# Performance work log

Measured on AMD Instinct MI355X. Metric: run time of the kernel, lower is better.

Reference implementation:

```python
import jax, jax.numpy as jnp
import numpy as np

MAXLEN = 256          # max per-graph segment length (static for jit)
SOFT_LABEL_NUM = 4    # hardcoded in the original module
B = 512               # num_graphs


def setup_inputs() -> dict:
    key = jax.random.key(0)
    k1, k2, k3 = jax.random.split(key, 3)
    # ragged per-graph lengths in [2, MAXLEN]; >=2 so the original's
    # length-1 skip path (and its cursor bug) never triggers
    s_num = jax.random.randint(k1, (B,), 2, MAXLEN + 1, dtype=jnp.int32)
    T = int(jnp.sum(s_num))
    logits = jax.random.normal(k2, (T,), dtype=jnp.float32)
    labels = jax.random.randint(k3, (T,), 0, SOFT_LABEL_NUM, dtype=jnp.int32)
    return {"logits": logits, "labels": labels, "s_num": s_num}


def reference(logits, labels, s_num):
    T = logits.shape[0]
    ends = jnp.cumsum(s_num)
    offsets = ends - s_num                                   # segment starts
    pos_in_seg = jnp.arange(MAXLEN)
    idx = jnp.clip(offsets[:, None] + pos_in_seg[None, :], 0, T - 1)  # [B, L]
    tok_mask = pos_in_seg[None, :] < s_num[:, None]                    # [B, L]

    lg = logits[idx]                                   # [B, L] padded logits
    lb = labels[idx]                                   # [B, L] padded labels

    # pairwise logsigmoid(pos - neg), computed once for all soft labels
    ls = jax.nn.log_sigmoid(lg[:, :, None] - lg[:, None, :])  # [B, L, L]

    means, valids = [], []
    for s in range(1, SOFT_LABEL_NUM):
        pos = (tok_mask & (lb == s)).astype(lg.dtype)  # [B, L]
        neg = (tok_mask & (lb < s)).astype(lg.dtype)   # [B, L]
        npos = pos.sum(-1)                             # [B]
        nneg = neg.sum(-1)                             # [B]
        pair_sum = jnp.einsum('bp,bpn,bn->b', pos, ls, neg)
        valid = (npos > 0) & (nneg > 0)
        mean_s = jnp.where(valid, pair_sum / jnp.maximum(npos * nneg, 1.0), 0.0)
        means.append(mean_s)
        valids.append(valid)

    means = jnp.stack(means)                 # [3, B]
    valids = jnp.stack(valids)               # [3, B]
    cnt = valids.astype(lg.dtype).sum(0)     # valid soft-label count per graph
    graph_valid = (s_num > 1) & (cnt > 0)
    graph_lp = jnp.where(graph_valid, means.sum(0) / jnp.maximum(cnt, 1.0), 0.0)
    n_valid = jnp.maximum(graph_valid.astype(lg.dtype).sum(), 1.0)
    loss = -(graph_lp.sum() / n_valid)
    return loss
```

## Files before the change

### kernel.cpp

```cpp
#include <hip/hip_runtime.h>
#include <hip/hip_bf16.h>


__global__ __launch_bounds__(256) void bpr_main(const float* __restrict__ logits,
                                                const int* __restrict__ labels,
                                                const int* __restrict__ s_num,
                                                int B,
                                                float* __restrict__ glp,
                                                float* __restrict__ flg) {
    const int b = blockIdx.x;
    const int t = threadIdx.x;

    __shared__ __align__(16) float se[256];
    __shared__ float sx[256];
    __shared__ float psum[4];
    __shared__ int   cnt[4];
    __shared__ int   cur[4];
    __shared__ int   wsum[4];

    if (t < 4) { psum[t] = 0.0f; cnt[t] = 0; cur[t] = 0; }
    se[t] = 0.0f;
    sx[t] = 0.0f;

    int partial = 0;
    for (int i = t; i < b; i += 256) partial += s_num[i];
    #pragma unroll
    for (int off = 32; off > 0; off >>= 1)
        partial += __shfl_down(partial, off, 64);
    if ((t & 63) == 0) wsum[t >> 6] = partial;
    __syncthreads();
    const int offset = wsum[0] + wsum[1] + wsum[2] + wsum[3];
    const int L = s_num[b];

    float x = 0.0f;
    int   l = 0;
    if (t < L) {
        x = logits[offset + t];
        l = labels[offset + t];
        atomicAdd(&cnt[l], 1);
    }
    __syncthreads();

    const int c0 = cnt[0], c1 = cnt[1], c2 = cnt[2];
    const int P1 = c0, P2 = c0 + c1, P3 = c0 + c1 + c2;

    if (t < L) {
        const int base = (l == 1) ? P1 : (l == 2) ? P2 : (l == 3) ? P3 : 0;
        const int pos  = base + atomicAdd(&cur[l], 1);
        se[pos] = __expf(x);
        sx[pos] = x;
    }
    __syncthreads();

    int si = 0;
    if (t < L) si = (t >= P1) + (t >= P2) + (t >= P3);
    const int C = (si == 1) ? P1 : (si == 2) ? P2 : (si == 3) ? P3 : 0;

    const float xi = sx[t];
    const float Ei = se[t];
    float acc2 = 0.0f;
    for (int j = 0; j < C; j += 8) {
        const float4 e0 = *reinterpret_cast<const float4*>(&se[j]);
        const float4 e1 = *reinterpret_cast<const float4*>(&se[j + 4]);
        acc2 += (j + 0 < C) ? __log2f(Ei + e0.x) : 0.0f;
        acc2 += (j + 1 < C) ? __log2f(Ei + e0.y) : 0.0f;
        acc2 += (j + 2 < C) ? __log2f(Ei + e0.z) : 0.0f;
        acc2 += (j + 3 < C) ? __log2f(Ei + e0.w) : 0.0f;
        acc2 += (j + 4 < C) ? __log2f(Ei + e1.x) : 0.0f;
        acc2 += (j + 5 < C) ? __log2f(Ei + e1.y) : 0.0f;
        acc2 += (j + 6 < C) ? __log2f(Ei + e1.z) : 0.0f;
        acc2 += (j + 7 < C) ? __log2f(Ei + e1.w) : 0.0f;
    }

    if (si > 0) {
        const float a = (float)C * xi - 0.69314718055994531f * acc2;
        atomicAdd(&psum[si], a);
    }
    __syncthreads();

    if (t == 0) {
        const int P[4] = {0, P1, P2, P3};
        float lp = 0.0f;
        int   c  = 0;
        #pragma unroll
        for (int s = 1; s < 4; ++s) {
            const int npos = cnt[s];
            const int nneg = P[s];
            if (npos > 0 && nneg > 0) {
                lp += psum[s] / ((float)npos * (float)nneg);
                ++c;
            }
        }
        const bool gv = (c > 0);
        glp[b] = gv ? lp / (float)c : 0.0f;
        flg[b] = gv ? 1.0f : 0.0f;
    }
}

__global__ __launch_bounds__(256) void bpr_reduce(const float* __restrict__ glp,
                                                  const float* __restrict__ flg,
                                                  int B, float* __restrict__ out) {
    const int t = threadIdx.x;
    float s = 0.0f, n = 0.0f;
    for (int i = t; i < B; i += 256) { s += glp[i]; n += flg[i]; }
    #pragma unroll
    for (int off = 32; off > 0; off >>= 1) {
        s += __shfl_down(s, off, 64);
        n += __shfl_down(n, off, 64);
    }
    __shared__ float ws[4], wn[4];
    if ((t & 63) == 0) { ws[t >> 6] = s; wn[t >> 6] = n; }
    __syncthreads();
    if (t == 0) {
        const float S = ws[0] + ws[1] + ws[2] + ws[3];
        const float N = wn[0] + wn[1] + wn[2] + wn[3];
        out[0] = -(S / fmaxf(N, 1.0f));
    }
}

extern "C" void kernel_launch(void* const* d_in, const int* in_sizes, int n_in,
                              void* d_out, int out_size, void* d_ws, size_t ws_size,
                              hipStream_t stream) {
    const float* logits = (const float*)d_in[0];
    const int*   labels = (const int*)d_in[1];
    const int*   s_num  = (const int*)d_in[2];
    const int B = in_sizes[2];

    float* glp = (float*)d_ws;
    float* flg = glp + B;

    bpr_main<<<B, 256, 0, stream>>>(logits, labels, s_num, B, glp, flg);
    bpr_reduce<<<1, 256, 0, stream>>>(glp, flg, B, (float*)d_out);
}
```

Measured before the change: 14.28 us.

## Split pairwise loop across four thread slices and use ballot-based label bucketing

Launches each graph block with 1024 threads so four 256-thread slices share the inner negative loop in a strided way, cutting per-thread serial log2 work. Shared-memory atomics for label counts and slot assignment are replaced by wave ballots and popcounts, and per-label partial sums are reduced with wave shuffles before one atomic per wave. The final reduce kernel reads with float4 loads. The larger blocks add barrier cost and reduce how many blocks fit per CU. Correctness depends on the rank-based slot order, and the stale shared entries past L are no longer zeroed.

```diff
diff --git a/kernel.cpp b/kernel.cpp
--- a/kernel.cpp
+++ b/kernel.cpp
@@ -2,97 +2,115 @@
 #include <hip/hip_bf16.h>
 
 
-__global__ __launch_bounds__(256) void bpr_main(const float* __restrict__ logits,
-                                                const int* __restrict__ labels,
-                                                const int* __restrict__ s_num,
-                                                int B,
-                                                float* __restrict__ glp,
-                                                float* __restrict__ flg) {
-    const int b = blockIdx.x;
-    const int t = threadIdx.x;
+__global__ __launch_bounds__(1024) void bpr_main(const float* __restrict__ logits,
+                                                 const int* __restrict__ labels,
+                                                 const int* __restrict__ s_num,
+                                                 int B,
+                                                 float* __restrict__ glp,
+                                                 float* __restrict__ flg) {
+    const int b  = blockIdx.x;
+    const int t  = threadIdx.x;
+    const int r  = t & 255;
+    const int sl = t >> 8;
+    const int w  = t >> 6;
+    const int lane = t & 63;
 
     __shared__ __align__(16) float se[256];
     __shared__ float sx[256];
     __shared__ float psum[4];
-    __shared__ int   cnt[4];
-    __shared__ int   cur[4];
+    __shared__ int   wcnt[4][4];
     __shared__ int   wsum[4];
 
-    if (t < 4) { psum[t] = 0.0f; cnt[t] = 0; cur[t] = 0; }
-    se[t] = 0.0f;
-    sx[t] = 0.0f;
+    if (t < 4) psum[t] = 0.0f;
 
-    int partial = 0;
-    for (int i = t; i < b; i += 256) partial += s_num[i];
-    #pragma unroll
-    for (int off = 32; off > 0; off >>= 1)
-        partial += __shfl_down(partial, off, 64);
-    if ((t & 63) == 0) wsum[t >> 6] = partial;
+    if (t < 256) {
+        int partial = 0;
+        for (int i = t; i < b; i += 256) partial += s_num[i];
+        #pragma unroll
+        for (int off = 32; off > 0; off >>= 1)
+            partial += __shfl_down(partial, off, 64);
+        if (lane == 0) wsum[w] = partial;
+    }
     __syncthreads();
     const int offset = wsum[0] + wsum[1] + wsum[2] + wsum[3];
     const int L = s_num[b];
 
     float x = 0.0f;
-    int   l = 0;
-    if (t < L) {
+    int   l = -1;
+    if (t < 256 && t < L) {
         x = logits[offset + t];
         l = labels[offset + t];
-        atomicAdd(&cnt[l], 1);
     }
+    const unsigned long long m0 = __ballot(l == 0);
+    const unsigned long long m1 = __ballot(l == 1);
+    const unsigned long long m2 = __ballot(l == 2);
+    const unsigned long long m3 = __ballot(l == 3);
+    if (w < 4 && lane == 0) {
+        wcnt[w][0] = __popcll(m0);
+        wcnt[w][1] = __popcll(m1);
+        wcnt[w][2] = __popcll(m2);
+        wcnt[w][3] = __popcll(m3);
+    }
+    const unsigned long long below = lane ? (~0ull >> (64 - lane)) : 0ull;
+    const unsigned long long mymask = (l == 0) ? m0 : (l == 1) ? m1 : (l == 2) ? m2 : m3;
+    const int rank = __popcll(mymask & below);
     __syncthreads();
 
-    const int c0 = cnt[0], c1 = cnt[1], c2 = cnt[2];
+    int c0 = wcnt[0][0] + wcnt[1][0] + wcnt[2][0] + wcnt[3][0];
+    int c1 = wcnt[0][1] + wcnt[1][1] + wcnt[2][1] + wcnt[3][1];
+    int c2 = wcnt[0][2] + wcnt[1][2] + wcnt[2][2] + wcnt[3][2];
+    int c3 = wcnt[0][3] + wcnt[1][3] + wcnt[2][3] + wcnt[3][3];
     const int P1 = c0, P2 = c0 + c1, P3 = c0 + c1 + c2;
 
-    if (t < L) {
-        const int base = (l == 1) ? P1 : (l == 2) ? P2 : (l == 3) ? P3 : 0;
-        const int pos  = base + atomicAdd(&cur[l], 1);
+    if (t < 256 && t < L) {
+        int base = (l == 0) ? 0 : (l == 1) ? P1 : (l == 2) ? P2 : P3;
+        for (int w2 = 0; w2 < w; ++w2) base += wcnt[w2][l];
+        const int pos = base + rank;
         se[pos] = __expf(x);
         sx[pos] = x;
     }
     __syncthreads();
 
     int si = 0;
-    if (t < L) si = (t >= P1) + (t >= P2) + (t >= P3);
+    if (r < L) si = (r >= P1) + (r >= P2) + (r >= P3);
     const int C = (si == 1) ? P1 : (si == 2) ? P2 : (si == 3) ? P3 : 0;
+    const float xi = sx[r];
+    const float Ei = se[r];
 
-    const float xi = sx[t];
-    const float Ei = se[t];
     float acc2 = 0.0f;
-    for (int j = 0; j < C; j += 8) {
+    for (int j = 8 * sl; j + 8 <= C; j += 32) {
         const float4 e0 = *reinterpret_cast<const float4*>(&se[j]);
         const float4 e1 = *reinterpret_cast<const float4*>(&se[j + 4]);
-        acc2 += (j + 0 < C) ? __log2f(Ei + e0.x) : 0.0f;
-        acc2 += (j + 1 < C) ? __log2f(Ei + e0.y) : 0.0f;
-        acc2 += (j + 2 < C) ? __log2f(Ei + e0.z) : 0.0f;
-        acc2 += (j + 3 < C) ? __log2f(Ei + e0.w) : 0.0f;
-        acc2 += (j + 4 < C) ? __log2f(Ei + e1.x) : 0.0f;
-        acc2 += (j + 5 < C) ? __log2f(Ei + e1.y) : 0.0f;
-        acc2 += (j + 6 < C) ? __log2f(Ei + e1.z) : 0.0f;
-        acc2 += (j + 7 < C) ? __log2f(Ei + e1.w) : 0.0f;
+        acc2 += __log2f(Ei + e0.x) + __log2f(Ei + e0.y)
+              + __log2f(Ei + e0.z) + __log2f(Ei + e0.w)
+              + __log2f(Ei + e1.x) + __log2f(Ei + e1.y)
+              + __log2f(Ei + e1.z) + __log2f(Ei + e1.w);
     }
+    const int jb = C & ~7;
+    if (si > 0 && sl == ((C >> 3) & 3)) {
+        for (int j = jb; j < C; ++j) acc2 += __log2f(Ei + se[j]);
+    }
+    float v = -0.69314718055994531f * acc2;
+    if (sl == 0 && si > 0) v += (float)C * xi;
 
-    if (si > 0) {
-        const float a = (float)C * xi - 0.69314718055994531f * acc2;
-        atomicAdd(&psum[si], a);
+    #pragma unroll
+    for (int s2 = 1; s2 < 4; ++s2) {
+        float val = (si == s2) ? v : 0.0f;
+        #pragma unroll
+        for (int off = 32; off > 0; off >>= 1)
+            val += __shfl_down(val, off, 64);
+        if (lane == 0 && val != 0.0f) atomicAdd(&psum[s2], val);
     }
     __syncthreads();
 
     if (t == 0) {
-        const int P[4] = {0, P1, P2, P3};
         float lp = 0.0f;
-        int   c  = 0;
-        #pragma unroll
-        for (int s = 1; s < 4; ++s) {
-            const int npos = cnt[s];
-            const int nneg = P[s];
-            if (npos > 0 && nneg > 0) {
-                lp += psum[s] / ((float)npos * (float)nneg);
-                ++c;
-            }
-        }
-        const bool gv = (c > 0);
-        glp[b] = gv ? lp / (float)c : 0.0f;
+        int   cc = 0;
+        if (c1 > 0 && P1 > 0) { lp += psum[1] / ((float)c1 * (float)P1); ++cc; }
+        if (c2 > 0 && P2 > 0) { lp += psum[2] / ((float)c2 * (float)P2); ++cc; }
+        if (c3 > 0 && P3 > 0) { lp += psum[3] / ((float)c3 * (float)P3); ++cc; }
+        const bool gv = (cc > 0);
+        glp[b] = gv ? lp / (float)cc : 0.0f;
         flg[b] = gv ? 1.0f : 0.0f;
     }
 }
@@ -101,19 +119,29 @@
                                                   const float* __restrict__ flg,
                                                   int B, float* __restrict__ out) {
     const int t = threadIdx.x;
+    const int lane = t & 63;
+    const int w = t >> 6;
+    const int n4 = B >> 2;
     float s = 0.0f, n = 0.0f;
-    for (int i = t; i < B; i += 256) { s += glp[i]; n += flg[i]; }
+    if (t < 128) {
+        const float4* g4 = (const float4*)glp;
+        for (int i = t; i < n4; i += 128) { float4 v = g4[i]; s += v.x + v.y + v.z + v.w; }
+        if (t == 0)   for (int i = n4 << 2; i < B; ++i) s += glp[i];
+    } else {
+        const float4* f4 = (const float4*)flg;
+        for (int i = t - 128; i < n4; i += 128) { float4 v = f4[i]; n += v.x + v.y + v.z + v.w; }
+        if (t == 128) for (int i = n4 << 2; i < B; ++i) n += flg[i];
+    }
+    float val = s + n;
     #pragma unroll
-    for (int off = 32; off > 0; off >>= 1) {
-        s += __shfl_down(s, off, 64);
-        n += __shfl_down(n, off, 64);
-    }
-    __shared__ float ws[4], wn[4];
-    if ((t & 63) == 0) { ws[t >> 6] = s; wn[t >> 6] = n; }
+    for (int off = 32; off > 0; off >>= 1)
+        val += __shfl_down(val, off, 64);
+    __shared__ float wred[4];
+    if (lane == 0) wred[w] = val;
     __syncthreads();
     if (t == 0) {
-        const float S = ws[0] + ws[1] + ws[2] + ws[3];
-        const float N = wn[0] + wn[1] + wn[2] + wn[3];
+        const float S = wred[0] + wred[1];
+        const float N = wred[2] + wred[3];
         out[0] = -(S / fmaxf(N, 1.0f));
     }
 }
@@ -129,6 +157,6 @@
     float* glp = (float*)d_ws;
     float* flg = glp + B;
 
-    bpr_main<<<B, 256, 0, stream>>>(logits, labels, s_num, B, glp, flg);
+    bpr_main<<<B, 1024, 0, stream>>>(logits, labels, s_num, B, glp, flg);
     bpr_reduce<<<1, 256, 0, stream>>>(glp, flg, B, (float*)d_out);
 }
```

Measured after the change: 13.81 us. 3.3% less time.
